# Optimization experiments

Measured on AMD Instinct MI355X. Metric: run time of the kernel, lower is better.

## Reference

```python
import jax, jax.numpy as jnp
import numpy as np

EPS = 1e-6
ROPE_THETA = 10000.0


def setup_inputs() -> dict:
    key = jax.random.key(0)
    ks = jax.random.split(key, 6)
    B, S, D = 2, 2048, 2048
    H, KVH, HD = 16, 4, 128
    hidden_states = jax.random.normal(ks[0], (B, S, D), dtype=jnp.float32)
    # RoPE tables (HF style: freqs duplicated across the two halves)
    inv_freq = 1.0 / (ROPE_THETA ** (jnp.arange(0, HD, 2, dtype=jnp.float32) / HD))
    pos = jnp.arange(S, dtype=jnp.float32)
    freqs = pos[:, None] * inv_freq[None, :]            # [S, HD/2]
    emb = jnp.concatenate([freqs, freqs], axis=-1)       # [S, HD]
    cos, sin = jnp.cos(emb), jnp.sin(emb)
    w_scale = 0.02
    q_w = jax.random.normal(ks[1], (H * HD, D), dtype=jnp.float32) * w_scale
    k_w = jax.random.normal(ks[2], (KVH * HD, D), dtype=jnp.float32) * w_scale
    v_w = jax.random.normal(ks[3], (KVH * HD, D), dtype=jnp.float32) * w_scale
    o_w = jax.random.normal(ks[4], (D, H * HD), dtype=jnp.float32) * w_scale
    q_norm_w = jnp.ones((HD,), dtype=jnp.float32)
    k_norm_w = jnp.ones((HD,), dtype=jnp.float32)
    return {
        "hidden_states": hidden_states, "cos": cos, "sin": sin,
        "q_w": q_w, "k_w": k_w, "v_w": v_w, "o_w": o_w,
        "q_norm_w": q_norm_w, "k_norm_w": k_norm_w,
    }


def _rms_norm(x, w):
    # Qwen3RMSNorm: fp32 variance, scale, cast back
    xf = x.astype(jnp.float32)
    var = jnp.mean(xf * xf, axis=-1, keepdims=True)
    out = xf * jax.lax.rsqrt(var + EPS)
    return (out * w.astype(jnp.float32)).astype(x.dtype)


def _rotate_half(x):
    half = x.shape[-1] // 2
    return jnp.concatenate([-x[..., half:], x[..., :half]], axis=-1)


def reference(hidden_states, cos, sin, q_w, k_w, v_w, o_w, q_norm_w, k_norm_w):
    B, S, D = hidden_states.shape
    HD = q_norm_w.shape[0]
    H = q_w.shape[0] // HD
    KVH = k_w.shape[0] // HD
    groups = H // KVH
    scale = HD ** -0.5

    # QKV projections (no bias) -> [B, heads, S, HD]
    q = (hidden_states @ q_w.T).reshape(B, S, H, HD)
    k = (hidden_states @ k_w.T).reshape(B, S, KVH, HD)
    v = (hidden_states @ v_w.T).reshape(B, S, KVH, HD)
    q = _rms_norm(q, q_norm_w).transpose(0, 2, 1, 3)   # [B,H,S,HD]
    k = _rms_norm(k, k_norm_w).transpose(0, 2, 1, 3)   # [B,KVH,S,HD]
    v = v.transpose(0, 2, 1, 3)                        # [B,KVH,S,HD]

    # RoPE (broadcast over batch and heads)
    c = cos[None, None, :, :]
    s = sin[None, None, :, :]
    q = q * c + _rotate_half(q) * s
    k = k * c + _rotate_half(k) * s

    # GQA expand kv heads
    if groups > 1:
        k = jnp.repeat(k, groups, axis=1)              # [B,H,S,HD]
        v = jnp.repeat(v, groups, axis=1)

    # SDPA, non-causal, no mask, no dropout
    scores = jnp.einsum("bhqd,bhkd->bhqk", q, k) * scale
    probs = jax.nn.softmax(scores, axis=-1)
    attn = jnp.einsum("bhqk,bhkd->bhqd", probs, v)     # [B,H,S,HD]

    attn = attn.transpose(0, 2, 1, 3).reshape(B, S, H * HD)
    return attn @ o_w.T
```

## Files before the change

### kernel.cpp

```cpp
#include <hip/hip_runtime.h>
#include <hip/hip_bf16.h>
#include <math.h>

#define B_   2
#define S_   2048
#define D_   2048
#define H_   16
#define KVH_ 4
#define HD_  128
#define SCALE 0.08838834764831845f
#define LOG2E 1.44269504088896f
#define EPS_  1e-6f

typedef unsigned short u16;
typedef unsigned int   u32;
typedef __attribute__((ext_vector_type(8)))  short bf16x8;
typedef __attribute__((ext_vector_type(4)))  float f32x4;
typedef __attribute__((ext_vector_type(16))) float f32x16;

__device__ __forceinline__ u16 f2bf(float x) {
    union { float f; unsigned int u; } v; v.f = x;
    unsigned int r = v.u + 0x7fffu + ((v.u >> 16) & 1u);
    return (u16)(r >> 16);
}
__device__ __forceinline__ float bf2f(u16 b) {
    union { float f; unsigned int u; } v; v.u = ((unsigned int)b) << 16;
    return v.f;
}
__device__ __forceinline__ u32 cvtpk(float lo, float hi) {
    u32 r;
    asm("v_cvt_pk_bf16_f32 %0, %1, %2" : "=v"(r) : "v"(lo), "v"(hi));
    return r;
}
__device__ __forceinline__ void gload16(const void* g, void* lds) {
    __builtin_amdgcn_global_load_lds(
        (const __attribute__((address_space(1))) unsigned int*)g,
        (__attribute__((address_space(3))) unsigned int*)lds, 16, 0, 0);
}

__global__ __launch_bounds__(256) void f2b_all(
    const float* __restrict__ s0, u16* __restrict__ d0, int n0,
    const float* __restrict__ s1, u16* __restrict__ d1, int n1,
    const float* __restrict__ s2, u16* __restrict__ d2, int n2,
    const float* __restrict__ s3, u16* __restrict__ d3, int n3,
    const float* __restrict__ s4, u16* __restrict__ d4, int n4)
{
    const float* s; u16* d; int n;
    switch (blockIdx.y) {
        case 0: s = s0; d = d0; n = n0; break;
        case 1: s = s1; d = d1; n = n1; break;
        case 2: s = s2; d = d2; n = n2; break;
        case 3: s = s3; d = d3; n = n3; break;
        default: s = s4; d = d4; n = n4; break;
    }
    int i = blockIdx.x * 256 + threadIdx.x;
    if (i >= n) return;
    float4 v = ((const float4*)s)[i];
    ushort4 o = make_ushort4(f2bf(v.x), f2bf(v.y), f2bf(v.z), f2bf(v.w));
    ((ushort4*)d)[i] = o;
}

template<int MODE>
__global__ __launch_bounds__(256) void gemm_bf16(
    const u16* __restrict__ A,
    const u16* __restrict__ Bw,
    u16* __restrict__ Qo, u16* __restrict__ Ko, u16* __restrict__ Vt,
    float* __restrict__ Co)
{
    __shared__ u16 As[128 * 64];
    __shared__ u16 Bs[128 * 64];

    const int t  = threadIdx.x;
    const int w  = t >> 6, l = t & 63;
    const int wm = w >> 1, wn = w & 1;
    const int lr = l & 15, lh = l >> 4;
    const int n0 = blockIdx.x * 128;
    const int m0 = blockIdx.y * 128;

    f32x4 acc[4][4];
    #pragma unroll
    for (int i = 0; i < 4; ++i)
        #pragma unroll
        for (int j = 0; j < 4; ++j)
            acc[i][j] = (f32x4)0.f;

    const int x = (w * 4) * 1024 + l * 16;
    for (int k0 = 0; k0 < 2048; k0 += 64) {
        #pragma unroll
        for (int u = 0; u < 4; ++u) {
            int xb = x + u * 1024;
            int r  = xb >> 7;
            int c  = xb & 127;
            int cs = c ^ ((r & 7) << 4);
            gload16(&A[(size_t)(m0 + r) * 2048 + k0 + (cs >> 1)], &As[(w * 4 + u) * 512]);
            gload16(&Bw[(size_t)(n0 + r) * 2048 + k0 + (cs >> 1)], &Bs[(w * 4 + u) * 512]);
        }
        __syncthreads();
        #pragma unroll
        for (int kc = 0; kc < 2; ++kc) {
            bf16x8 af[4], bfr[4];
            #pragma unroll
            for (int i = 0; i < 4; ++i) {
                int row = wm * 64 + i * 16 + lr;
                int byt = row * 128 + ((kc * 64 + lh * 16) ^ ((row & 7) << 4));
                af[i] = *(const bf16x8*)&As[byt >> 1];
                int rob = wn * 64 + i * 16 + lr;
                int byb = rob * 128 + ((kc * 64 + lh * 16) ^ ((rob & 7) << 4));
                bfr[i] = *(const bf16x8*)&Bs[byb >> 1];
            }
            #pragma unroll
            for (int i = 0; i < 4; ++i)
                #pragma unroll
                for (int j = 0; j < 4; ++j)
                    acc[i][j] = __builtin_amdgcn_mfma_f32_16x16x32_bf16(
                        af[i], bfr[j], acc[i][j], 0, 0, 0);
        }
        __syncthreads();
    }

    #pragma unroll
    for (int i = 0; i < 4; ++i) {
        #pragma unroll
        for (int j = 0; j < 4; ++j) {
            int col = n0 + wn * 64 + j * 16 + lr;
            #pragma unroll
            for (int r = 0; r < 4; ++r) {
                int m = m0 + wm * 64 + i * 16 + lh * 4 + r;
                float v = acc[i][j][r];
                if (MODE == 0) {
                    int bb = m >> 11, s = m & 2047;
                    if (col < 2048) {
                        int hh = col >> 7, d = col & 127;
                        Qo[((size_t)(bb * H_ + hh) * S_ + s) * HD_ + d] = f2bf(v);
                    } else if (col < 2560) {
                        int c2 = col - 2048; int hh = c2 >> 7, d = c2 & 127;
                        Ko[((size_t)(bb * KVH_ + hh) * S_ + s) * HD_ + d] = f2bf(v);
                    } else {
                        int c2 = col - 2560; int hh = c2 >> 7, d = c2 & 127;
                        Vt[((size_t)(bb * KVH_ + hh) * HD_ + d) * S_ + s] = f2bf(v);
                    }
                } else {
                    Co[(size_t)m * 2048 + col] = v;
                }
            }
        }
    }
}

__global__ __launch_bounds__(256) void norm_rope(
    u16* __restrict__ Qb, u16* __restrict__ Kb,
    const float* __restrict__ cosb, const float* __restrict__ sinb,
    const float* __restrict__ qnw, const float* __restrict__ knw)
{
    const int rid = blockIdx.x * 4 + (threadIdx.x >> 6);
    const int l   = threadIdx.x & 63;
    u16* row; const float* wn; int s; float sc;
    if (rid < B_ * H_ * S_) {
        row = Qb + (size_t)rid * HD_; wn = qnw; s = rid & (S_ - 1); sc = SCALE * LOG2E;
    } else {
        int r2 = rid - B_ * H_ * S_;
        row = Kb + (size_t)r2 * HD_; wn = knw; s = r2 & (S_ - 1); sc = 1.f;
    }
    unsigned int u = *(const unsigned int*)&row[2 * l];
    float x0 = bf2f((u16)(u & 0xffff)), x1 = bf2f((u16)(u >> 16));
    float ss = x0 * x0 + x1 * x1;
    #pragma unroll
    for (int off = 1; off < 64; off <<= 1) ss += __shfl_xor(ss, off);
    float rr = rsqrtf(ss * (1.f / 128.f) + 1e-6f);
    float n0 = x0 * rr * wn[2 * l];
    float n1 = x1 * rr * wn[2 * l + 1];
    float p0 = __shfl_xor(n0, 32);
    float p1 = __shfl_xor(n1, 32);
    float sg = (l < 32) ? -1.f : 1.f;
    const float* cp = cosb + s * HD_;
    const float* sp = sinb + s * HD_;
    float o0 = (n0 * cp[2 * l]     + sg * p0 * sp[2 * l])     * sc;
    float o1 = (n1 * cp[2 * l + 1] + sg * p1 * sp[2 * l + 1]) * sc;
    unsigned int o = (unsigned int)f2bf(o0) | ((unsigned int)f2bf(o1) << 16);
    *(unsigned int*)&row[2 * l] = o;
}

__global__ __launch_bounds__(256, 2) void attn_mfma(
    const u16* __restrict__ Q,
    const u16* __restrict__ K,
    const u16* __restrict__ Vt,
    u16* __restrict__ AO)
{
    __shared__ u16 Ks[2][64 * 128];
    __shared__ u16 Vs[2][128 * 64];

    const int t  = threadIdx.x, w = t >> 6, l = t & 63;
    const int lq = l & 31, hi = l >> 5;
    const int id = (blockIdx.x & 7) * 64 + (blockIdx.x >> 3);
    const int qx = id & 15, bh = id >> 4;
    const int bb = bh >> 4, h = bh & 15;
    const int kv = bb * KVH_ + (h >> 2);
    const int q0 = qx * 128 + w * 32;

    const u16* Qp = Q + ((size_t)bh * S_ + q0) * HD_;
    const u16* Kp = K + (size_t)kv * S_ * HD_;
    const u16* Vp = Vt + (size_t)kv * HD_ * S_;

    bf16x8 aq[8];
    #pragma unroll
    for (int ks = 0; ks < 8; ++ks)
        aq[ks] = *(const bf16x8*)&Qp[(size_t)lq * 128 + ks * 16 + hi * 8];

    const u16* kptr[4];
    const u16* vptr[4];
    #pragma unroll
    for (int u = 0; u < 4; ++u) {
        int xb = (w * 4 + u) * 1024 + l * 16;
        int rk = xb >> 8, ck = xb & 255;
        kptr[u] = &Kp[(size_t)rk * 128 + ((ck ^ ((rk & 7) << 4)) >> 1)];
        int rv = xb >> 7, cv = xb & 127;
        vptr[u] = &Vp[(size_t)rv * S_ + ((cv ^ ((rv & 7) << 4)) >> 1)];
    }

    f32x16 oacc[4];
    #pragma unroll
    for (int dt = 0; dt < 4; ++dt) oacc[dt] = (f32x16)0.f;
    float mrun = -1e30f, lrun = 0.f;

    auto stage = [&](int buf) {
        #pragma unroll
        for (int u = 0; u < 4; ++u) {
            gload16(kptr[u], &Ks[buf][(w * 4 + u) * 512]);
            gload16(vptr[u], &Vs[buf][(w * 4 + u) * 512]);
            kptr[u] += 64 * 128;
            vptr[u] += 64;
        }
    };

    stage(0);
    __syncthreads();

    const int NT = S_ / 64;
    #pragma unroll 2
    for (int kt = 0; kt < NT; ++kt) {
        const int cur = kt & 1;
        if (kt + 1 < NT) stage(cur ^ 1);

        f32x16 sacc[2];
        sacc[0] = (f32x16)0.f; sacc[1] = (f32x16)0.f;
        __builtin_amdgcn_s_setprio(1);
        #pragma unroll
        for (int kb = 0; kb < 2; ++kb) {
            #pragma unroll
            for (int ks = 0; ks < 8; ++ks) {
                int row = kb * 32 + lq;
                int byt = row * 256 + ((ks * 32 + hi * 16) ^ ((row & 7) << 4));
                bf16x8 kf = *(const bf16x8*)&Ks[cur][byt >> 1];
                sacc[kb] = __builtin_amdgcn_mfma_f32_32x32x16_bf16(
                    kf, aq[ks], sacc[kb], 0, 0, 0);
            }
        }
        __builtin_amdgcn_s_setprio(0);

        float mx = -1e30f;
        #pragma unroll
        for (int r = 0; r < 16; ++r)
            mx = fmaxf(mx, fmaxf(sacc[0][r], sacc[1][r]));
        mx = fmaxf(mx, __shfl_xor(mx, 32));
        if (__any(mx > mrun + 8.f)) {
            float mn = fmaxf(mrun, mx);
            float al = __builtin_exp2f(mrun - mn);
            mrun = mn;
            lrun *= al;
            #pragma unroll
            for (int r = 0; r < 16; ++r) {
                int src = (r & 3) + 8 * (r >> 2) + 4 * hi;
                float alr = __shfl(al, src);
                #pragma unroll
                for (int dt = 0; dt < 4; ++dt) oacc[dt][r] *= alr;
            }
        }
        float ps = 0.f;
        #pragma unroll
        for (int kb = 0; kb < 2; ++kb)
            #pragma unroll
            for (int r = 0; r < 16; ++r) {
                float p = __builtin_exp2f(sacc[kb][r] - mrun);
                sacc[kb][r] = p;
                ps += p;
            }
        ps += __shfl_xor(ps, 32);
        lrun += ps;

        #pragma unroll
        for (int kb = 0; kb < 2; ++kb) {
            u32 wv[8], sv[8];
            #pragma unroll
            for (int i = 0; i < 8; ++i)
                wv[i] = cvtpk(sacc[kb][2 * i], sacc[kb][2 * i + 1]);
            #pragma unroll
            for (int i = 0; i < 8; ++i)
                sv[i] = __shfl_xor(wv[i], 32);
            #pragma unroll
            for (int k2 = 0; k2 < 2; ++k2) {
                union { u32 u[4]; bf16x8 v; } pa;
                pa.u[0] = hi ? sv[4 * k2 + 2] : wv[4 * k2 + 0];
                pa.u[1] = hi ? sv[4 * k2 + 3] : wv[4 * k2 + 1];
                pa.u[2] = hi ? wv[4 * k2 + 2] : sv[4 * k2 + 0];
                pa.u[3] = hi ? wv[4 * k2 + 3] : sv[4 * k2 + 1];
                int kloc = (kb * 2 + k2) * 16 + hi * 8;
                __builtin_amdgcn_s_setprio(1);
                #pragma unroll
                for (int dt = 0; dt < 4; ++dt) {
                    int rowv = dt * 32 + lq;
                    int byv  = rowv * 128 + ((kloc * 2) ^ ((rowv & 7) << 4));
                    bf16x8 vf = *(const bf16x8*)&Vs[cur][byv >> 1];
                    oacc[dt] = __builtin_amdgcn_mfma_f32_32x32x16_bf16(
                        pa.v, vf, oacc[dt], 0, 0, 0);
                }
                __builtin_amdgcn_s_setprio(0);
            }
        }
        __syncthreads();
    }

    #pragma unroll
    for (int r = 0; r < 16; ++r) {
        int src = (r & 3) + 8 * (r >> 2) + 4 * hi;
        float linv = 1.f / __shfl(lrun, src);
        int s = q0 + src;
        size_t base = ((size_t)bb * S_ + s) * 2048 + h * 128 + lq;
        #pragma unroll
        for (int dt = 0; dt < 4; ++dt)
            AO[base + dt * 32] = f2bf(oacc[dt][r] * linv);
    }
}

extern "C" void kernel_launch(void* const* d_in, const int* in_sizes, int n_in,
                              void* d_out, int out_size, void* d_ws, size_t ws_size,
                              hipStream_t stream) {
    (void)in_sizes; (void)n_in; (void)out_size; (void)ws_size;
    const float* hid  = (const float*)d_in[0];
    const float* cosb = (const float*)d_in[1];
    const float* sinb = (const float*)d_in[2];
    const float* qw   = (const float*)d_in[3];
    const float* kw   = (const float*)d_in[4];
    const float* vw   = (const float*)d_in[5];
    const float* ow   = (const float*)d_in[6];
    const float* qnw  = (const float*)d_in[7];
    const float* knw  = (const float*)d_in[8];

    u16* ws   = (u16*)d_ws;
    u16* hidB = ws;
    u16* Wc   = ws + 8388608;
    u16* owB  = ws + 14680064;
    u16* Qb   = ws + 18874368;
    u16* Kb   = ws + 27262976;
    u16* VtB  = ws + 29360128;
    u16* AO   = ws + 31457280;

    f2b_all<<<dim3(8192, 5), 256, 0, stream>>>(
        hid, hidB, 2097152,
        qw,  Wc,            1048576,
        kw,  Wc + 4194304,  262144,
        vw,  Wc + 5242880,  262144,
        ow,  owB,           1048576);

    gemm_bf16<0><<<dim3(24, 32), 256, 0, stream>>>(hidB, Wc, Qb, Kb, VtB, nullptr);
    norm_rope<<<20480, 256, 0, stream>>>(Qb, Kb, cosb, sinb, qnw, knw);
    attn_mfma<<<512, 256, 0, stream>>>(Qb, Kb, VtB, AO);
    gemm_bf16<1><<<dim3(16, 32), 256, 0, stream>>>(AO, owB, nullptr, nullptr, nullptr,
                                                   (float*)d_out);
}
```

Baseline: 243.0 us.

## Use permlane32_swap for P fragment exchange and recompute K/V load addresses

Replaces the 8 __shfl_xor (ds_bpermute-based) lane exchanges and select logic for building the P operand with v_permlane32_swap instructions. Drops the persistent per-lane K/V pointer arrays and computes load addresses from the tile offset, which lowers register pressure. Also removes the s_setprio priority bumps around the MFMA blocks and the unroll-2 pragma on the main loop. These aim to cut LDS-path shuffle traffic and VGPR use, at the cost of extra address arithmetic per stage and the loss of scheduling priority hints.

Result: faster. 237.0 us (-2.5%).

```diff
diff --git a/kernel.cpp b/kernel.cpp
--- a/kernel.cpp
+++ b/kernel.cpp
@@ -14,6 +14,7 @@
 
 typedef unsigned short u16;
 typedef unsigned int   u32;
+typedef __attribute__((ext_vector_type(2)))  unsigned int u32x2;
 typedef __attribute__((ext_vector_type(8)))  short bf16x8;
 typedef __attribute__((ext_vector_type(4)))  float f32x4;
 typedef __attribute__((ext_vector_type(16))) float f32x16;
@@ -206,44 +207,34 @@
     for (int ks = 0; ks < 8; ++ks)
         aq[ks] = *(const bf16x8*)&Qp[(size_t)lq * 128 + ks * 16 + hi * 8];
 
-    const u16* kptr[4];
-    const u16* vptr[4];
-    #pragma unroll
-    for (int u = 0; u < 4; ++u) {
-        int xb = (w * 4 + u) * 1024 + l * 16;
-        int rk = xb >> 8, ck = xb & 255;
-        kptr[u] = &Kp[(size_t)rk * 128 + ((ck ^ ((rk & 7) << 4)) >> 1)];
-        int rv = xb >> 7, cv = xb & 127;
-        vptr[u] = &Vp[(size_t)rv * S_ + ((cv ^ ((rv & 7) << 4)) >> 1)];
-    }
-
     f32x16 oacc[4];
     #pragma unroll
     for (int dt = 0; dt < 4; ++dt) oacc[dt] = (f32x16)0.f;
     float mrun = -1e30f, lrun = 0.f;
 
-    auto stage = [&](int buf) {
+    auto stage = [&](int k0, int buf) {
         #pragma unroll
         for (int u = 0; u < 4; ++u) {
-            gload16(kptr[u], &Ks[buf][(w * 4 + u) * 512]);
-            gload16(vptr[u], &Vs[buf][(w * 4 + u) * 512]);
-            kptr[u] += 64 * 128;
-            vptr[u] += 64;
+            int xb = (w * 4 + u) * 1024 + l * 16;
+            int rk = xb >> 8, ck = xb & 255;
+            gload16(&Kp[(size_t)(k0 + rk) * 128 + ((ck ^ ((rk & 7) << 4)) >> 1)],
+                    &Ks[buf][(w * 4 + u) * 512]);
+            int rv = xb >> 7, cv = xb & 127;
+            gload16(&Vp[(size_t)rv * S_ + k0 + ((cv ^ ((rv & 7) << 4)) >> 1)],
+                    &Vs[buf][(w * 4 + u) * 512]);
         }
     };
 
-    stage(0);
+    stage(0, 0);
     __syncthreads();
 
     const int NT = S_ / 64;
-    #pragma unroll 2
     for (int kt = 0; kt < NT; ++kt) {
         const int cur = kt & 1;
-        if (kt + 1 < NT) stage(cur ^ 1);
+        if (kt + 1 < NT) stage((kt + 1) * 64, cur ^ 1);
 
         f32x16 sacc[2];
         sacc[0] = (f32x16)0.f; sacc[1] = (f32x16)0.f;
-        __builtin_amdgcn_s_setprio(1);
         #pragma unroll
         for (int kb = 0; kb < 2; ++kb) {
             #pragma unroll
@@ -255,7 +246,6 @@
                     kf, aq[ks], sacc[kb], 0, 0, 0);
             }
         }
-        __builtin_amdgcn_s_setprio(0);
 
         float mx = -1e30f;
         #pragma unroll
@@ -289,22 +279,20 @@
 
         #pragma unroll
         for (int kb = 0; kb < 2; ++kb) {
-            u32 wv[8], sv[8];
+            u32 wv[8];
             #pragma unroll
             for (int i = 0; i < 8; ++i)
                 wv[i] = cvtpk(sacc[kb][2 * i], sacc[kb][2 * i + 1]);
             #pragma unroll
-            for (int i = 0; i < 8; ++i)
-                sv[i] = __shfl_xor(wv[i], 32);
-            #pragma unroll
             for (int k2 = 0; k2 < 2; ++k2) {
+                u32x2 r0 = __builtin_amdgcn_permlane32_swap(
+                    wv[4 * k2 + 0], wv[4 * k2 + 2], false, false);
+                u32x2 r1 = __builtin_amdgcn_permlane32_swap(
+                    wv[4 * k2 + 1], wv[4 * k2 + 3], false, false);
                 union { u32 u[4]; bf16x8 v; } pa;
-                pa.u[0] = hi ? sv[4 * k2 + 2] : wv[4 * k2 + 0];
-                pa.u[1] = hi ? sv[4 * k2 + 3] : wv[4 * k2 + 1];
-                pa.u[2] = hi ? wv[4 * k2 + 2] : sv[4 * k2 + 0];
-                pa.u[3] = hi ? wv[4 * k2 + 3] : sv[4 * k2 + 1];
+                pa.u[0] = r0.x; pa.u[1] = r1.x;
+                pa.u[2] = r0.y; pa.u[3] = r1.y;
                 int kloc = (kb * 2 + k2) * 16 + hi * 8;
-                __builtin_amdgcn_s_setprio(1);
                 #pragma unroll
                 for (int dt = 0; dt < 4; ++dt) {
                     int rowv = dt * 32 + lq;
@@ -313,7 +301,6 @@
                     oacc[dt] = __builtin_amdgcn_mfma_f32_32x32x16_bf16(
                         pa.v, vf, oacc[dt], 0, 0, 0);
                 }
-                __builtin_amdgcn_s_setprio(0);
             }
         }
         __syncthreads();
```
